# Kernel optimization log

Measured on AMD Instinct MI355X. Metric: run time of the kernel, lower is better.

Reference implementation:

```python
import jax, jax.numpy as jnp
import numpy as np


def setup_inputs() -> dict:
    key = jax.random.key(0)
    ks = jax.random.split(key, 4)
    B, C, H, W = 8, 64, 256, 256
    return {
        "x": jax.random.normal(ks[0], (B, C, H, W), jnp.float32),
        "fc_w": jax.random.normal(ks[1], (C, C), jnp.float32) / np.sqrt(C).astype(np.float32),
        "fc_b": jnp.zeros((C,), jnp.float32),
        "conv1_w": jax.random.normal(ks[2], (2,), jnp.float32),  # [mean_ch, max_ch] of 1x1 conv
        "conv1_b": jnp.zeros((1,), jnp.float32),
        "conv2_w": jax.random.normal(ks[3], (2,), jnp.float32),
        "conv2_b": jnp.zeros((1,), jnp.float32),
        "size": 4,
    }


def reference(x, fc_w, fc_b, conv1_w, conv1_b, conv2_w, conv2_b, size):
    B, C, H, W = x.shape
    s = size
    h, w = H // s, W // s
    # unfold (non-overlapping) -> [B, L, C, s*s], L = h*w, patch pixels row-major
    p = x.reshape(B, C, h, s, w, s).transpose(0, 2, 4, 1, 3, 5).reshape(B, h * w, C, s * s)
    # channel attention: max over patch pixels -> fc -> sigmoid
    m = jax.nn.sigmoid(jnp.max(p, axis=3) @ fc_w.T + fc_b)  # [B, L, C]
    p = p * m[..., None]
    # spatial-in-patch attention: (mean, max) over channel axis -> 1x1 conv(2->1) -> sigmoid
    g1 = jax.nn.sigmoid(
        conv1_w[0] * jnp.mean(p, axis=2, keepdims=True)
        + conv1_w[1] * jnp.max(p, axis=2, keepdims=True)
        + conv1_b[0]
    )  # [B, L, 1, s*s]
    p = p * g1
    # fold back to [B, C, H, W]
    y = p.reshape(B, h, w, C, s, s).transpose(0, 3, 1, 4, 2, 5).reshape(B, C, H, W)
    # per-patch gating: (mean, max) over all C*s*s values of each patch
    yb = y.reshape(B, C, h, s, w, s)
    mx = jnp.max(yb, axis=(1, 3, 5))   # [B, h, w]
    mn = jnp.mean(yb, axis=(1, 3, 5))  # [B, h, w]
    g2 = jax.nn.sigmoid(conv2_w[0] * mn + conv2_w[1] * mx + conv2_b[0])
    g2 = jnp.repeat(jnp.repeat(g2, s, axis=1), s, axis=2)  # [B, H, W]
    return y * g2[:, None, :, :]
```

## Files before the change

### kernel.cpp

```cpp
#include <hip/hip_runtime.h>
#include <math.h>

constexpr int Bc = 8, Cc = 64, Hc = 256, Wc = 256, Sc = 4;
constexpr int NPATCH = Bc * (Hc / Sc) * (Wc / Sc);
constexpr int TP = 8;
constexpr int CPITCH = 133;
constexpr int RPITCH = 33;

__device__ __forceinline__ float sigmoidf_(float v) {
    return 1.0f / (1.0f + __expf(-v));
}

__global__ __launch_bounds__(256, 2)
void ciam_kernel(const float* __restrict__ x,
                 const float* __restrict__ fc_w,
                 const float* __restrict__ fc_b,
                 const float* __restrict__ c1w,
                 const float* __restrict__ c1b,
                 const float* __restrict__ c2w,
                 const float* __restrict__ c2b,
                 float* __restrict__ out)
{
    __shared__ float T[64 * CPITCH];
    __shared__ float fcw_lds[64 * 65];
    __shared__ float maxbuf[TP][64];
    __shared__ float pixbuf[4][16 * 65];
    __shared__ float g1buf[4][2][16];

    const int tid  = threadIdx.x;
    const int gid  = blockIdx.x;
    const int b    = gid >> 9;
    const int rem  = gid & 511;
    const int ph   = rem >> 3;
    const int pwg  = rem & 7;
    const int col0 = pwg * 32;

    #pragma unroll
    for (int i = 0; i < 4; ++i) {
        int u   = i * 256 + tid;
        int row = u >> 4;
        int jf  = (u & 15) << 2;
        const float4 wv = *reinterpret_cast<const float4*>(fc_w + row * 64 + jf);
        float* fd = &fcw_lds[row * 65 + jf];
        fd[0] = wv.x; fd[1] = wv.y; fd[2] = wv.z; fd[3] = wv.w;
    }

    #pragma unroll
    for (int i = 0; i < 8; ++i) {
        int u   = i * 256 + tid;
        int seg = u >> 3;
        int c_  = seg >> 2;
        int r_  = seg & 3;
        int j4  = (u & 7) << 2;
        const float4 val = *reinterpret_cast<const float4*>(
            x + (((size_t)(b * Cc + c_) * Hc + (ph * Sc + r_)) * Wc + col0 + j4));
        float* td = &T[c_ * CPITCH + r_ * RPITCH + j4];
        td[0] = val.x; td[1] = val.y; td[2] = val.z; td[3] = val.w;
    }

    const float w10 = c1w[0], w11 = c1w[1], b1 = c1b[0];
    const float w20 = c2w[0], w21 = c2w[1], b2 = c2b[0];

    __syncthreads();

    const int wave = tid >> 6;
    const int lane = tid & 63;
    const int c    = lane;
    const int p0   = wave * 2;

    float v[2][16];
    #pragma unroll
    for (int pi = 0; pi < 2; ++pi) {
        const float* tp = &T[c * CPITCH + (p0 + pi) * 4];
        #pragma unroll
        for (int r = 0; r < 4; ++r)
            #pragma unroll
            for (int j = 0; j < 4; ++j)
                v[pi][r * 4 + j] = tp[r * RPITCH + j];
    }

    float mx0 = -3.4e38f, mx1 = -3.4e38f;
    #pragma unroll
    for (int t = 0; t < 16; ++t) {
        mx0 = fmaxf(mx0, v[0][t]);
        mx1 = fmaxf(mx1, v[1][t]);
    }
    maxbuf[p0][c]     = mx0;
    maxbuf[p0 + 1][c] = mx1;
    __syncthreads();

    float a0 = fc_b[c], a1 = a0;
    #pragma unroll 16
    for (int k = 0; k < 64; ++k) {
        float wv = fcw_lds[c * 65 + k];
        a0 = fmaf(wv, maxbuf[p0][k], a0);
        a1 = fmaf(wv, maxbuf[p0 + 1][k], a1);
    }
    const float m0 = sigmoidf_(a0), m1 = sigmoidf_(a1);
    #pragma unroll
    for (int t = 0; t < 16; ++t) { v[0][t] *= m0; v[1][t] *= m1; }

    #pragma unroll
    for (int pi = 0; pi < 2; ++pi) {
        #pragma unroll
        for (int t = 0; t < 16; ++t)
            pixbuf[wave][t * 65 + c] = v[pi][t];
        __syncthreads();
        {
            const int a = lane >> 2, q = lane & 3;
            const float* pb = &pixbuf[wave][a * 65 + q * 16];
            float s = 0.f, mxp = -3.4e38f;
            #pragma unroll
            for (int t = 0; t < 16; ++t) {
                float u = pb[t];
                s += u;
                mxp = fmaxf(mxp, u);
            }
            s   += __shfl_xor(s, 1);
            s   += __shfl_xor(s, 2);
            mxp  = fmaxf(mxp, __shfl_xor(mxp, 1));
            mxp  = fmaxf(mxp, __shfl_xor(mxp, 2));
            float g1 = sigmoidf_(w10 * (s * (1.f / 64.f)) + w11 * mxp + b1);
            if (q == 0) g1buf[wave][pi][a] = g1;
        }
        __syncthreads();
        #pragma unroll
        for (int t = 0; t < 16; ++t)
            v[pi][t] *= g1buf[wave][pi][t];
    }

    #pragma unroll
    for (int pi = 0; pi < 2; ++pi) {
        float ls = 0.f, lmx = -3.4e38f;
        #pragma unroll
        for (int t = 0; t < 16; ++t) {
            ls += v[pi][t];
            lmx = fmaxf(lmx, v[pi][t]);
        }
        #pragma unroll
        for (int off = 32; off >= 1; off >>= 1) {
            ls  += __shfl_xor(ls, off);
            lmx  = fmaxf(lmx, __shfl_xor(lmx, off));
        }
        const float g2 = sigmoidf_(w20 * (ls * (1.f / 1024.f)) + w21 * lmx + b2);
        float* tp = &T[c * CPITCH + (p0 + pi) * 4];
        #pragma unroll
        for (int r = 0; r < 4; ++r)
            #pragma unroll
            for (int j = 0; j < 4; ++j)
                tp[r * RPITCH + j] = v[pi][r * 4 + j] * g2;
    }
    __syncthreads();

    #pragma unroll
    for (int i = 0; i < 8; ++i) {
        int u   = i * 256 + tid;
        int seg = u >> 3;
        int c_  = seg >> 2;
        int r_  = seg & 3;
        int j4  = (u & 7) << 2;
        const float* ts = &T[c_ * CPITCH + r_ * RPITCH + j4];
        float4 o;
        o.x = ts[0]; o.y = ts[1]; o.z = ts[2]; o.w = ts[3];
        *reinterpret_cast<float4*>(
            out + (((size_t)(b * Cc + c_) * Hc + (ph * Sc + r_)) * Wc + col0 + j4)) = o;
    }
}

extern "C" void kernel_launch(void* const* d_in, const int* in_sizes, int n_in,
                              void* d_out, int out_size, void* d_ws, size_t ws_size,
                              hipStream_t stream) {
    const float* x    = (const float*)d_in[0];
    const float* fc_w = (const float*)d_in[1];
    const float* fc_b = (const float*)d_in[2];
    const float* c1w  = (const float*)d_in[3];
    const float* c1b  = (const float*)d_in[4];
    const float* c2w  = (const float*)d_in[5];
    const float* c2b  = (const float*)d_in[6];

    float* out = (float*)d_out;
    ciam_kernel<<<NPATCH / TP, 256, 0, stream>>>(x, fc_w, fc_b, c1w, c1b, c2w, c2b, out);
}
```

Baseline: 258.6 us.

## Overlay LDS buffers, raise occupancy, fuse gating reductions and store directly

Shrinks shared memory by overlaying the fc weight and pixel buffers inside the tile region, and raises launch bounds to four blocks per CU. Global loads are issued into registers up front, and LDS accesses use float4/float2. The per-patch gate reductions are derived from the per-pixel sum/max scaled by the positive g1, which removes a full reduction pass and several block barriers. Outputs are written straight from registers, which replaces the coalesced LDS-staged store with per-lane 16-byte row writes. Intra-wave syncing relies on s_waitcnt instead of __syncthreads.

Result: slower. 278.8 us (+7.8%).

```diff
diff --git a/kernel.cpp b/kernel.cpp
--- a/kernel.cpp
+++ b/kernel.cpp
@@ -4,14 +4,23 @@
 constexpr int Bc = 8, Cc = 64, Hc = 256, Wc = 256, Sc = 4;
 constexpr int NPATCH = Bc * (Hc / Sc) * (Wc / Sc);
 constexpr int TP = 8;
-constexpr int CPITCH = 133;
-constexpr int RPITCH = 33;
+
+constexpr int RP = 36;
+constexpr int CP = 4 * RP + 4;
+constexpr int TILE_F = Cc * CP;
+
+constexpr int FCW_P   = 66;
+constexpr int FCW_OFF = 0;
+constexpr int PIX_P   = 68;
+constexpr int PIX_OFF = Cc * FCW_P;
+constexpr int PIX_W   = 16 * PIX_P;
+static_assert(PIX_OFF + 4 * PIX_W <= TILE_F, "overlay must fit inside tile");
 
 __device__ __forceinline__ float sigmoidf_(float v) {
     return 1.0f / (1.0f + __expf(-v));
 }
 
-__global__ __launch_bounds__(256, 2)
+__global__ __launch_bounds__(256, 4)
 void ciam_kernel(const float* __restrict__ x,
                  const float* __restrict__ fc_w,
                  const float* __restrict__ fc_b,
@@ -21,11 +30,8 @@
                  const float* __restrict__ c2b,
                  float* __restrict__ out)
 {
-    __shared__ float T[64 * CPITCH];
-    __shared__ float fcw_lds[64 * 65];
-    __shared__ float maxbuf[TP][64];
-    __shared__ float pixbuf[4][16 * 65];
-    __shared__ float g1buf[4][2][16];
+    __shared__ __align__(16) float S[TILE_F];
+    __shared__ __align__(16) float maxbuf[TP][64];
 
     const int tid  = threadIdx.x;
     const int gid  = blockIdx.x;
@@ -35,48 +41,46 @@
     const int pwg  = rem & 7;
     const int col0 = pwg * 32;
 
+    float4 tl[8];
+    #pragma unroll
+    for (int i = 0; i < 8; ++i) {
+        const int u = i * 256 + tid;
+        const int seg = u >> 3, c_ = seg >> 2, r_ = seg & 3, j4 = (u & 7) << 2;
+        tl[i] = *reinterpret_cast<const float4*>(
+            x + (((size_t)(b * Cc + c_) * Hc + (ph * Sc + r_)) * Wc + col0 + j4));
+    }
+    float4 wl[4];
     #pragma unroll
     for (int i = 0; i < 4; ++i) {
-        int u   = i * 256 + tid;
-        int row = u >> 4;
-        int jf  = (u & 15) << 2;
-        const float4 wv = *reinterpret_cast<const float4*>(fc_w + row * 64 + jf);
-        float* fd = &fcw_lds[row * 65 + jf];
-        fd[0] = wv.x; fd[1] = wv.y; fd[2] = wv.z; fd[3] = wv.w;
+        const int u = i * 256 + tid;
+        const int row = u >> 4, jf = (u & 15) << 2;
+        wl[i] = *reinterpret_cast<const float4*>(fc_w + row * 64 + jf);
     }
+    const float fb  = fc_b[tid & 63];
+    const float w10 = c1w[0], w11 = c1w[1], b1 = c1b[0];
+    const float w20 = c2w[0], w21 = c2w[1], b2 = c2b[0];
 
     #pragma unroll
     for (int i = 0; i < 8; ++i) {
-        int u   = i * 256 + tid;
-        int seg = u >> 3;
-        int c_  = seg >> 2;
-        int r_  = seg & 3;
-        int j4  = (u & 7) << 2;
-        const float4 val = *reinterpret_cast<const float4*>(
-            x + (((size_t)(b * Cc + c_) * Hc + (ph * Sc + r_)) * Wc + col0 + j4));
-        float* td = &T[c_ * CPITCH + r_ * RPITCH + j4];
-        td[0] = val.x; td[1] = val.y; td[2] = val.z; td[3] = val.w;
+        const int u = i * 256 + tid;
+        const int seg = u >> 3, c_ = seg >> 2, r_ = seg & 3, j4 = (u & 7) << 2;
+        *reinterpret_cast<float4*>(&S[c_ * CP + r_ * RP + j4]) = tl[i];
     }
-
-    const float w10 = c1w[0], w11 = c1w[1], b1 = c1b[0];
-    const float w20 = c2w[0], w21 = c2w[1], b2 = c2b[0];
-
     __syncthreads();
 
-    const int wave = tid >> 6;
-    const int lane = tid & 63;
-    const int c    = lane;
-    const int p0   = wave * 2;
+    const int wave = tid >> 6, lane = tid & 63, c = lane;
+    const int p0 = wave * 2;
 
     float v[2][16];
     #pragma unroll
     for (int pi = 0; pi < 2; ++pi) {
-        const float* tp = &T[c * CPITCH + (p0 + pi) * 4];
+        const float* tp = &S[c * CP + (p0 + pi) * 4];
         #pragma unroll
-        for (int r = 0; r < 4; ++r)
-            #pragma unroll
-            for (int j = 0; j < 4; ++j)
-                v[pi][r * 4 + j] = tp[r * RPITCH + j];
+        for (int r = 0; r < 4; ++r) {
+            const float4 q4 = *reinterpret_cast<const float4*>(tp + r * RP);
+            v[pi][r*4+0] = q4.x; v[pi][r*4+1] = q4.y;
+            v[pi][r*4+2] = q4.z; v[pi][r*4+3] = q4.w;
+        }
     }
 
     float mx0 = -3.4e38f, mx1 = -3.4e38f;
@@ -89,81 +93,73 @@
     maxbuf[p0 + 1][c] = mx1;
     __syncthreads();
 
-    float a0 = fc_b[c], a1 = a0;
-    #pragma unroll 16
-    for (int k = 0; k < 64; ++k) {
-        float wv = fcw_lds[c * 65 + k];
-        a0 = fmaf(wv, maxbuf[p0][k], a0);
-        a1 = fmaf(wv, maxbuf[p0 + 1][k], a1);
+    #pragma unroll
+    for (int i = 0; i < 4; ++i) {
+        const int u = i * 256 + tid;
+        const int row = u >> 4, jf = (u & 15) << 2;
+        float* fd = &S[FCW_OFF + row * FCW_P + jf];
+        fd[0] = wl[i].x; fd[1] = wl[i].y; fd[2] = wl[i].z; fd[3] = wl[i].w;
+    }
+    __syncthreads();
+
+    const float* wrow = &S[FCW_OFF + c * FCW_P];
+    const float* m0r  = maxbuf[p0];
+    const float* m1r  = maxbuf[p0 + 1];
+    float a0 = fb, a1 = fb;
+    #pragma unroll 8
+    for (int k2 = 0; k2 < 32; ++k2) {
+        const float2 wv = *reinterpret_cast<const float2*>(wrow + 2 * k2);
+        const float2 q0 = *reinterpret_cast<const float2*>(m0r + 2 * k2);
+        const float2 q1 = *reinterpret_cast<const float2*>(m1r + 2 * k2);
+        a0 = fmaf(wv.x, q0.x, a0); a0 = fmaf(wv.y, q0.y, a0);
+        a1 = fmaf(wv.x, q1.x, a1); a1 = fmaf(wv.y, q1.y, a1);
     }
     const float m0 = sigmoidf_(a0), m1 = sigmoidf_(a1);
     #pragma unroll
     for (int t = 0; t < 16; ++t) { v[0][t] *= m0; v[1][t] *= m1; }
 
+    float* PB = &S[PIX_OFF + wave * PIX_W];
+    const int a_ = lane >> 2, q_ = lane & 3;
+    const float* pbr = PB + a_ * PIX_P + q_ * 16;
+
     #pragma unroll
     for (int pi = 0; pi < 2; ++pi) {
         #pragma unroll
         for (int t = 0; t < 16; ++t)
-            pixbuf[wave][t * 65 + c] = v[pi][t];
-        __syncthreads();
-        {
-            const int a = lane >> 2, q = lane & 3;
-            const float* pb = &pixbuf[wave][a * 65 + q * 16];
-            float s = 0.f, mxp = -3.4e38f;
-            #pragma unroll
-            for (int t = 0; t < 16; ++t) {
-                float u = pb[t];
-                s += u;
-                mxp = fmaxf(mxp, u);
-            }
-            s   += __shfl_xor(s, 1);
-            s   += __shfl_xor(s, 2);
-            mxp  = fmaxf(mxp, __shfl_xor(mxp, 1));
-            mxp  = fmaxf(mxp, __shfl_xor(mxp, 2));
-            float g1 = sigmoidf_(w10 * (s * (1.f / 64.f)) + w11 * mxp + b1);
-            if (q == 0) g1buf[wave][pi][a] = g1;
+            PB[t * PIX_P + c] = v[pi][t];
+        __asm__ volatile("s_waitcnt lgkmcnt(0)" ::: "memory");
+
+        float s = 0.f, mxp = -3.4e38f;
+        #pragma unroll
+        for (int t4 = 0; t4 < 4; ++t4) {
+            const float4 u4 = *reinterpret_cast<const float4*>(pbr + 4 * t4);
+            s += (u4.x + u4.y) + (u4.z + u4.w);
+            mxp = fmaxf(mxp, fmaxf(fmaxf(u4.x, u4.y), fmaxf(u4.z, u4.w)));
         }
-        __syncthreads();
+        s += __shfl_xor(s, 1);
+        s += __shfl_xor(s, 2);
+        mxp = fmaxf(mxp, __shfl_xor(mxp, 1));
+        mxp = fmaxf(mxp, __shfl_xor(mxp, 2));
+        const float g1 = sigmoidf_(w10 * (s * (1.f / 64.f)) + w11 * mxp + b1);
+
+        float ts = g1 * s, tm = g1 * mxp;
         #pragma unroll
-        for (int t = 0; t < 16; ++t)
-            v[pi][t] *= g1buf[wave][pi][t];
-    }
+        for (int off = 4; off <= 32; off <<= 1) {
+            ts += __shfl_xor(ts, off);
+            tm  = fmaxf(tm, __shfl_xor(tm, off));
+        }
+        const float g2 = sigmoidf_(w20 * (ts * (1.f / 1024.f)) + w21 * tm + b2);
 
-    #pragma unroll
-    for (int pi = 0; pi < 2; ++pi) {
-        float ls = 0.f, lmx = -3.4e38f;
+        const size_t obase = ((size_t)(b * Cc + c) * Hc + ph * Sc) * Wc + col0 + (p0 + pi) * 4;
         #pragma unroll
-        for (int t = 0; t < 16; ++t) {
-            ls += v[pi][t];
-            lmx = fmaxf(lmx, v[pi][t]);
+        for (int r = 0; r < 4; ++r) {
+            float4 o;
+            o.x = v[pi][r*4+0] * (__shfl(g1, (r*4+0) << 2) * g2);
+            o.y = v[pi][r*4+1] * (__shfl(g1, (r*4+1) << 2) * g2);
+            o.z = v[pi][r*4+2] * (__shfl(g1, (r*4+2) << 2) * g2);
+            o.w = v[pi][r*4+3] * (__shfl(g1, (r*4+3) << 2) * g2);
+            *reinterpret_cast<float4*>(out + obase + (size_t)r * Wc) = o;
         }
-        #pragma unroll
-        for (int off = 32; off >= 1; off >>= 1) {
-            ls  += __shfl_xor(ls, off);
-            lmx  = fmaxf(lmx, __shfl_xor(lmx, off));
-        }
-        const float g2 = sigmoidf_(w20 * (ls * (1.f / 1024.f)) + w21 * lmx + b2);
-        float* tp = &T[c * CPITCH + (p0 + pi) * 4];
-        #pragma unroll
-        for (int r = 0; r < 4; ++r)
-            #pragma unroll
-            for (int j = 0; j < 4; ++j)
-                tp[r * RPITCH + j] = v[pi][r * 4 + j] * g2;
-    }
-    __syncthreads();
-
-    #pragma unroll
-    for (int i = 0; i < 8; ++i) {
-        int u   = i * 256 + tid;
-        int seg = u >> 3;
-        int c_  = seg >> 2;
-        int r_  = seg & 3;
-        int j4  = (u & 7) << 2;
-        const float* ts = &T[c_ * CPITCH + r_ * RPITCH + j4];
-        float4 o;
-        o.x = ts[0]; o.y = ts[1]; o.z = ts[2]; o.w = ts[3];
-        *reinterpret_cast<float4*>(
-            out + (((size_t)(b * Cc + c_) * Hc + (ph * Sc + r_)) * Wc + col0 + j4)) = o;
     }
 }
 
```
